# Optimization experiments

Measured on AMD Instinct MI355X. Metric: run time of the kernel, lower is better.

The kernel has to match this reference:

```python
import jax, jax.numpy as jnp
import numpy as np

NUM_PIXELS, B, C, H, A = 4096, 64, 512, 512, 256


def setup_inputs() -> dict:
    key = jax.random.key(0)
    ks = jax.random.split(key, 8)
    s = 0.02
    return {
        "keys": jax.random.normal(ks[0], (NUM_PIXELS, B, C), jnp.float32),
        "queries": jax.random.normal(ks[1], (1, B, H), jnp.float32),
        "Wa_w": jax.random.normal(ks[2], (A, C), jnp.float32) * s,
        "Wa_b": jax.random.normal(ks[3], (A,), jnp.float32) * s,
        "Ua_w": jax.random.normal(ks[4], (A, H), jnp.float32) * s,
        "Ua_b": jax.random.normal(ks[5], (A,), jnp.float32) * s,
        "va_w": jax.random.normal(ks[6], (1, A), jnp.float32) * s,
        "va_b": jax.random.normal(ks[7], (1,), jnp.float32) * s,
    }


def reference(keys, queries, Wa_w, Wa_b, Ua_w, Ua_b, va_w, va_b):
    # attn1: [P, B, A]; attn2: [1, B, A]
    attn1 = jnp.einsum("pbc,ac->pba", keys, Wa_w) + Wa_b
    attn2 = jnp.einsum("qbh,ah->qba", queries, Ua_w) + Ua_b
    # scores: [P, B] (va projects attn_size -> 1)
    scores = jnp.einsum("pba,a->pb", jnp.tanh(attn1 + attn2), va_w[0]) + va_b[0]
    weights = jax.nn.softmax(scores, axis=0)[..., None]  # [P, B, 1]
    context = jnp.sum(weights * keys, axis=0, keepdims=True)  # [1, B, C]
    return (context, weights)
```

## Files before the change

kernel.cpp:

```cpp
#include <hip/hip_runtime.h>
#include <cstdint>

#define CC 512
#define AA 256

typedef __bf16 bf16x8 __attribute__((ext_vector_type(8)));
typedef float f32x16 __attribute__((ext_vector_type(16)));

__device__ __forceinline__ unsigned short f2bf(float f) {
  union { float f; uint32_t u; } v; v.f = f;
  uint32_t r = (v.u + 0x7FFFu + ((v.u >> 16) & 1u)) >> 16;
  return (unsigned short)r;
}

__global__ void prep_kernel(const float* __restrict__ q,
                            const float* __restrict__ Wa_w,
                            const float* __restrict__ Wa_b,
                            const float* __restrict__ Ua_w,
                            const float* __restrict__ Ua_b,
                            unsigned short* __restrict__ wa_bf,
                            float* __restrict__ attn2,
                            float* __restrict__ out_ctx) {
  const int blk = blockIdx.x, t = threadIdx.x;
  if (blk < 64) {
    const int b = blk, a = t;
    float acc = Ua_b[a] + Wa_b[a];
    const float4* qr = (const float4*)(q + (size_t)b * CC);
    const float4* ur = (const float4*)(Ua_w + (size_t)a * CC);
#pragma unroll 4
    for (int i = 0; i < CC / 4; ++i) {
      float4 uu = ur[i]; float4 qq = qr[i];
      acc += uu.x * qq.x + uu.y * qq.y + uu.z * qq.z + uu.w * qq.w;
    }
    attn2[b * AA + a] = acc;
  } else if (blk < 128) {
    const int base = (blk - 64) * 2048 + t * 8;
#pragma unroll
    for (int i = 0; i < 8; ++i) wa_bf[base + i] = f2bf(Wa_w[base + i]);
  } else {
    const int base = (blk - 128) * 512 + t * 2;
    out_ctx[base] = 0.f; out_ctx[base + 1] = 0.f;
  }
}

__global__ __launch_bounds__(256, 2) void scores_kernel(
    const float* __restrict__ keys,
    const unsigned short* __restrict__ wa_bf,
    const float* __restrict__ attn2,
    const float* __restrict__ va_w,
    const float* __restrict__ va_b,
    float* __restrict__ scores) {
  __shared__ __align__(16) unsigned char smem[55296];
  unsigned short* As = (unsigned short*)smem;
  unsigned short* Bs = As + 128 * 72;

  const int t = threadIdx.x;
  const int w = t >> 6, lane = t & 63;
  const int m32 = lane & 31, kg = lane >> 5;
  const int R0w = (w & 1) * 64, C0w = (w >> 1) * 128;
  const long r0 = (long)blockIdx.x * 128;

  f32x16 acc[2][4];
#pragma unroll
  for (int i = 0; i < 2; ++i)
#pragma unroll
    for (int j = 0; j < 4; ++j)
#pragma unroll
      for (int e = 0; e < 16; ++e) acc[i][j][e] = 0.f;

  const int c4 = t & 15, rg = t >> 4;
  const int kq = t & 7, ng = t >> 3;

  for (int ko = 0; ko < 8; ++ko) {
    const int kb = ko * 64;
#pragma unroll
    for (int ps = 0; ps < 8; ++ps) {
      const int row = rg + ps * 16;
      float4 v = *(const float4*)(keys + (r0 + row) * CC + kb + c4 * 4);
      ushort4 h;
      h.x = f2bf(v.x); h.y = f2bf(v.y); h.z = f2bf(v.z); h.w = f2bf(v.w);
      *(ushort4*)(As + row * 72 + c4 * 4) = h;
    }
#pragma unroll
    for (int ps = 0; ps < 8; ++ps) {
      const int n = ng + ps * 32;
      int4 v = *(const int4*)(wa_bf + (size_t)n * CC + kb + kq * 8);
      *(int4*)(Bs + n * 72 + kq * 8) = v;
    }
    __syncthreads();
    for (int kk = 0; kk < 4; ++kk) {
      const int k0 = kk * 16 + kg * 8;
      bf16x8 a0 = *(const bf16x8*)(As + (R0w + m32) * 72 + k0);
      bf16x8 a1 = *(const bf16x8*)(As + (R0w + 32 + m32) * 72 + k0);
      bf16x8 b0 = *(const bf16x8*)(Bs + (C0w + m32) * 72 + k0);
      bf16x8 b1 = *(const bf16x8*)(Bs + (C0w + 32 + m32) * 72 + k0);
      bf16x8 b2 = *(const bf16x8*)(Bs + (C0w + 64 + m32) * 72 + k0);
      bf16x8 b3 = *(const bf16x8*)(Bs + (C0w + 96 + m32) * 72 + k0);
      acc[0][0] = __builtin_amdgcn_mfma_f32_32x32x16_bf16(a0, b0, acc[0][0], 0, 0, 0);
      acc[0][1] = __builtin_amdgcn_mfma_f32_32x32x16_bf16(a0, b1, acc[0][1], 0, 0, 0);
      acc[0][2] = __builtin_amdgcn_mfma_f32_32x32x16_bf16(a0, b2, acc[0][2], 0, 0, 0);
      acc[0][3] = __builtin_amdgcn_mfma_f32_32x32x16_bf16(a0, b3, acc[0][3], 0, 0, 0);
      acc[1][0] = __builtin_amdgcn_mfma_f32_32x32x16_bf16(a1, b0, acc[1][0], 0, 0, 0);
      acc[1][1] = __builtin_amdgcn_mfma_f32_32x32x16_bf16(a1, b1, acc[1][1], 0, 0, 0);
      acc[1][2] = __builtin_amdgcn_mfma_f32_32x32x16_bf16(a1, b2, acc[1][2], 0, 0, 0);
      acc[1][3] = __builtin_amdgcn_mfma_f32_32x32x16_bf16(a1, b3, acc[1][3], 0, 0, 0);
    }
    __syncthreads();
  }

  float* sc0 = (float*)smem;
  float* sc1 = sc0 + 128;

#pragma unroll
  for (int mt = 0; mt < 2; ++mt) {
    float ps[16];
#pragma unroll
    for (int r = 0; r < 16; ++r) ps[r] = 0.f;
    const int rowb = R0w + mt * 32 + 4 * kg;
#pragma unroll
    for (int nt = 0; nt < 4; ++nt) {
      const int col = C0w + nt * 32 + m32;
      const float vv = va_w[col];
#pragma unroll
      for (int r = 0; r < 16; ++r) {
        const int row = rowb + (r & 3) + 8 * (r >> 2);
        float x = acc[mt][nt][r] + attn2[(row & 63) * AA + col];
        float ax = fabsf(x);
        float e2 = __expf(-2.f * ax);
        float th = (1.f - e2) / (1.f + e2);
        ps[r] += copysignf(th, x) * vv;
      }
    }
#pragma unroll
    for (int off = 1; off <= 16; off <<= 1)
#pragma unroll
      for (int r = 0; r < 16; ++r) ps[r] += __shfl_xor(ps[r], off);
    if (m32 == 0) {
      float* dst = (w >> 1) ? sc1 : sc0;
#pragma unroll
      for (int r = 0; r < 16; ++r) dst[rowb + (r & 3) + 8 * (r >> 2)] = ps[r];
    }
  }
  __syncthreads();
  if (t < 128) scores[r0 + t] = sc0[t] + sc1[t] + va_b[0];
}

__global__ void softmax_kernel(const float* __restrict__ scores,
                               float* __restrict__ out) {
  const int b = blockIdx.x, t = threadIdx.x;
  const int w = t >> 6, lane = t & 63;
  __shared__ float red[4];
  float s[16];
  float m = -1e30f;
#pragma unroll
  for (int i = 0; i < 16; ++i) {
    s[i] = scores[(size_t)(t + 256 * i) * 64 + b];
    m = fmaxf(m, s[i]);
  }
#pragma unroll
  for (int off = 1; off <= 32; off <<= 1) m = fmaxf(m, __shfl_xor(m, off));
  if (lane == 0) red[w] = m;
  __syncthreads();
  m = fmaxf(fmaxf(red[0], red[1]), fmaxf(red[2], red[3]));
  float sum = 0.f;
#pragma unroll
  for (int i = 0; i < 16; ++i) { s[i] = __expf(s[i] - m); sum += s[i]; }
#pragma unroll
  for (int off = 1; off <= 32; off <<= 1) sum += __shfl_xor(sum, off);
  __syncthreads();
  if (lane == 0) red[w] = sum;
  __syncthreads();
  const float invZ = 1.f / (red[0] + red[1] + red[2] + red[3]);
  float* wout = out + 32768;
#pragma unroll
  for (int i = 0; i < 16; ++i)
    wout[(size_t)(t + 256 * i) * 64 + b] = s[i] * invZ;
}

__global__ __launch_bounds__(128) void context_kernel(
    const float* __restrict__ keys,
    const float* __restrict__ wts,
    float* __restrict__ out_ctx) {
  const int b = blockIdx.y, pc = blockIdx.x, t = threadIdx.x;
  const int p0 = pc * 128;
  __shared__ float wl[128];
  wl[t] = wts[(size_t)(p0 + t) * 64 + b];
  __syncthreads();
  float4 acc = {0.f, 0.f, 0.f, 0.f};
  const float4* kp = (const float4*)keys;
#pragma unroll 4
  for (int j = 0; j < 128; ++j) {
    float4 kv = kp[(size_t)((p0 + j) * 64 + b) * 128 + t];
    const float wj = wl[j];
    acc.x += wj * kv.x; acc.y += wj * kv.y;
    acc.z += wj * kv.z; acc.w += wj * kv.w;
  }
  float* dst = out_ctx + b * 512 + t * 4;
  atomicAdd(dst + 0, acc.x);
  atomicAdd(dst + 1, acc.y);
  atomicAdd(dst + 2, acc.z);
  atomicAdd(dst + 3, acc.w);
}

extern "C" void kernel_launch(void* const* d_in, const int* in_sizes, int n_in,
                              void* d_out, int out_size, void* d_ws, size_t ws_size,
                              hipStream_t stream) {
  (void)in_sizes; (void)n_in; (void)out_size; (void)ws_size;
  const float* keys = (const float*)d_in[0];
  const float* q    = (const float*)d_in[1];
  const float* Wa_w = (const float*)d_in[2];
  const float* Wa_b = (const float*)d_in[3];
  const float* Ua_w = (const float*)d_in[4];
  const float* Ua_b = (const float*)d_in[5];
  const float* va_w = (const float*)d_in[6];
  const float* va_b = (const float*)d_in[7];
  float* out = (float*)d_out;

  unsigned short* wa_bf = (unsigned short*)d_ws;
  float* attn2  = (float*)((char*)d_ws + 262144);
  float* scores = (float*)((char*)d_ws + 262144 + 65536);

  prep_kernel<<<192, 256, 0, stream>>>(q, Wa_w, Wa_b, Ua_w, Ua_b, wa_bf, attn2, out);
  scores_kernel<<<2048, 256, 0, stream>>>(keys, wa_bf, attn2, va_w, va_b, scores);
  softmax_kernel<<<64, 256, 0, stream>>>(scores, out);
  context_kernel<<<dim3(32, 64), 128, 0, stream>>>(keys, out + 32768, out);
}
```

Measured before the change: 849.8 us.

## Fuse scores, unnormalized softmax and context accumulation into one persistent pass

Merges the score GEMM, exponentiation and weighted context sum into a single kernel. Each of 256 blocks processes 8 row tiles and accumulates per-block context partials while the keys are still hot, replacing the separate max-softmax and second full read of keys. The max subtraction is dropped and exp(score) is used directly, which relies on scores staying small enough not to overflow. The trade-offs are a 64-float per-thread register accumulator, a 32 MB partial buffer that needs a reduce pass, and 512-thread blocks with only 256 blocks.

Result: slower. 960.6 us (+13.0%).

```diff
diff --git a/kernel.cpp b/kernel.cpp
--- a/kernel.cpp
+++ b/kernel.cpp
@@ -3,14 +3,15 @@
 
 #define CC 512
 #define AA 256
+#define NBLK 256
+#define TPB 8
 
 typedef __bf16 bf16x8 __attribute__((ext_vector_type(8)));
 typedef float f32x16 __attribute__((ext_vector_type(16)));
 
 __device__ __forceinline__ unsigned short f2bf(float f) {
   union { float f; uint32_t u; } v; v.f = f;
-  uint32_t r = (v.u + 0x7FFFu + ((v.u >> 16) & 1u)) >> 16;
-  return (unsigned short)r;
+  return (unsigned short)((v.u + 0x7FFFu + ((v.u >> 16) & 1u)) >> 16);
 }
 
 __global__ void prep_kernel(const float* __restrict__ q,
@@ -19,8 +20,7 @@
                             const float* __restrict__ Ua_w,
                             const float* __restrict__ Ua_b,
                             unsigned short* __restrict__ wa_bf,
-                            float* __restrict__ attn2,
-                            float* __restrict__ out_ctx) {
+                            float* __restrict__ attn2) {
   const int blk = blockIdx.x, t = threadIdx.x;
   if (blk < 64) {
     const int b = blk, a = t;
@@ -29,177 +29,192 @@
     const float4* ur = (const float4*)(Ua_w + (size_t)a * CC);
 #pragma unroll 4
     for (int i = 0; i < CC / 4; ++i) {
-      float4 uu = ur[i]; float4 qq = qr[i];
+      float4 uu = ur[i], qq = qr[i];
       acc += uu.x * qq.x + uu.y * qq.y + uu.z * qq.z + uu.w * qq.w;
     }
     attn2[b * AA + a] = acc;
-  } else if (blk < 128) {
+  } else {
     const int base = (blk - 64) * 2048 + t * 8;
 #pragma unroll
     for (int i = 0; i < 8; ++i) wa_bf[base + i] = f2bf(Wa_w[base + i]);
-  } else {
-    const int base = (blk - 128) * 512 + t * 2;
-    out_ctx[base] = 0.f; out_ctx[base + 1] = 0.f;
-  }
-}
-
-__global__ __launch_bounds__(256, 2) void scores_kernel(
+  }
+}
+
+__global__ __launch_bounds__(512, 2) void fused_kernel(
     const float* __restrict__ keys,
     const unsigned short* __restrict__ wa_bf,
     const float* __restrict__ attn2,
     const float* __restrict__ va_w,
     const float* __restrict__ va_b,
-    float* __restrict__ scores) {
-  __shared__ __align__(16) unsigned char smem[55296];
-  unsigned short* As = (unsigned short*)smem;
-  unsigned short* Bs = As + 128 * 72;
+    float* __restrict__ u_g,
+    float* __restrict__ cpart,
+    float* __restrict__ zpart) {
+  __shared__ __align__(16) unsigned short As[128 * 72];
+  __shared__ __align__(16) unsigned short Bs[256 * 72];
+  __shared__ float sc[4][128];
+  __shared__ __align__(16) float u_s[128];
+  __shared__ float zp_s[64];
 
   const int t = threadIdx.x;
-  const int w = t >> 6, lane = t & 63;
-  const int m32 = lane & 31, kg = lane >> 5;
-  const int R0w = (w & 1) * 64, C0w = (w >> 1) * 128;
-  const long r0 = (long)blockIdx.x * 128;
-
-  f32x16 acc[2][4];
-#pragma unroll
-  for (int i = 0; i < 2; ++i)
-#pragma unroll
-    for (int j = 0; j < 4; ++j)
-#pragma unroll
-      for (int e = 0; e < 16; ++e) acc[i][j][e] = 0.f;
+  const int w = t >> 6, lane = t & 63, m32 = lane & 31, kg = lane >> 5;
+  const int R0w = (w & 1) * 64, C0w = (w >> 1) * 64;
+
+  float Cown[64];
+#pragma unroll
+  for (int b = 0; b < 64; ++b) Cown[b] = 0.f;
+  if (t < 64) zp_s[t] = 0.f;
+  __syncthreads();
 
   const int c4 = t & 15, rg = t >> 4;
   const int kq = t & 7, ng = t >> 3;
 
-  for (int ko = 0; ko < 8; ++ko) {
-    const int kb = ko * 64;
-#pragma unroll
-    for (int ps = 0; ps < 8; ++ps) {
-      const int row = rg + ps * 16;
-      float4 v = *(const float4*)(keys + (r0 + row) * CC + kb + c4 * 4);
-      ushort4 h;
-      h.x = f2bf(v.x); h.y = f2bf(v.y); h.z = f2bf(v.z); h.w = f2bf(v.w);
-      *(ushort4*)(As + row * 72 + c4 * 4) = h;
-    }
-#pragma unroll
-    for (int ps = 0; ps < 8; ++ps) {
-      const int n = ng + ps * 32;
-      int4 v = *(const int4*)(wa_bf + (size_t)n * CC + kb + kq * 8);
-      *(int4*)(Bs + n * 72 + kq * 8) = v;
+  for (int tile = 0; tile < TPB; ++tile) {
+    const long r0 = ((long)blockIdx.x * TPB + tile) * 128;
+
+    f32x16 acc[2][2];
+#pragma unroll
+    for (int i = 0; i < 2; ++i)
+#pragma unroll
+      for (int j = 0; j < 2; ++j)
+#pragma unroll
+        for (int e = 0; e < 16; ++e) acc[i][j][e] = 0.f;
+
+    for (int ko = 0; ko < 8; ++ko) {
+      const int kb = ko * 64;
+#pragma unroll
+      for (int ps = 0; ps < 4; ++ps) {
+        const int row = rg + ps * 32;
+        float4 v = *(const float4*)(keys + (size_t)(r0 + row) * CC + kb + c4 * 4);
+        ushort4 h;
+        h.x = f2bf(v.x); h.y = f2bf(v.y); h.z = f2bf(v.z); h.w = f2bf(v.w);
+        *(ushort4*)(As + row * 72 + c4 * 4) = h;
+      }
+#pragma unroll
+      for (int ps = 0; ps < 4; ++ps) {
+        const int n = ng + ps * 64;
+        int4 v = *(const int4*)(wa_bf + (size_t)n * CC + kb + kq * 8);
+        *(int4*)(Bs + n * 72 + kq * 8) = v;
+      }
+      __syncthreads();
+#pragma unroll
+      for (int kk = 0; kk < 4; ++kk) {
+        const int k0 = kk * 16 + kg * 8;
+        bf16x8 a0 = *(const bf16x8*)(As + (R0w + m32) * 72 + k0);
+        bf16x8 a1 = *(const bf16x8*)(As + (R0w + 32 + m32) * 72 + k0);
+        bf16x8 b0 = *(const bf16x8*)(Bs + (C0w + m32) * 72 + k0);
+        bf16x8 b1 = *(const bf16x8*)(Bs + (C0w + 32 + m32) * 72 + k0);
+        acc[0][0] = __builtin_amdgcn_mfma_f32_32x32x16_bf16(a0, b0, acc[0][0], 0, 0, 0);
+        acc[0][1] = __builtin_amdgcn_mfma_f32_32x32x16_bf16(a0, b1, acc[0][1], 0, 0, 0);
+        acc[1][0] = __builtin_amdgcn_mfma_f32_32x32x16_bf16(a1, b0, acc[1][0], 0, 0, 0);
+        acc[1][1] = __builtin_amdgcn_mfma_f32_32x32x16_bf16(a1, b1, acc[1][1], 0, 0, 0);
+      }
+      __syncthreads();
+    }
+
+#pragma unroll
+    for (int mt = 0; mt < 2; ++mt) {
+      float ps_[16];
+#pragma unroll
+      for (int r = 0; r < 16; ++r) ps_[r] = 0.f;
+      const int rowb = R0w + mt * 32 + 4 * kg;
+#pragma unroll
+      for (int nt = 0; nt < 2; ++nt) {
+        const int col = C0w + nt * 32 + m32;
+        const float vv = va_w[col];
+#pragma unroll
+        for (int r = 0; r < 16; ++r) {
+          const int row = rowb + (r & 3) + 8 * (r >> 2);
+          float x = acc[mt][nt][r] + attn2[(row & 63) * AA + col];
+          float ax = fabsf(x);
+          float e2 = __expf(-2.f * ax);
+          float th = (1.f - e2) / (1.f + e2);
+          ps_[r] += copysignf(th, x) * vv;
+        }
+      }
+#pragma unroll
+      for (int off = 1; off <= 16; off <<= 1)
+#pragma unroll
+        for (int r = 0; r < 16; ++r) ps_[r] += __shfl_xor(ps_[r], off);
+      if (m32 == 0) {
+#pragma unroll
+        for (int r = 0; r < 16; ++r)
+          sc[w >> 1][rowb + (r & 3) + 8 * (r >> 2)] = ps_[r];
+      }
     }
     __syncthreads();
-    for (int kk = 0; kk < 4; ++kk) {
-      const int k0 = kk * 16 + kg * 8;
-      bf16x8 a0 = *(const bf16x8*)(As + (R0w + m32) * 72 + k0);
-      bf16x8 a1 = *(const bf16x8*)(As + (R0w + 32 + m32) * 72 + k0);
-      bf16x8 b0 = *(const bf16x8*)(Bs + (C0w + m32) * 72 + k0);
-      bf16x8 b1 = *(const bf16x8*)(Bs + (C0w + 32 + m32) * 72 + k0);
-      bf16x8 b2 = *(const bf16x8*)(Bs + (C0w + 64 + m32) * 72 + k0);
-      bf16x8 b3 = *(const bf16x8*)(Bs + (C0w + 96 + m32) * 72 + k0);
-      acc[0][0] = __builtin_amdgcn_mfma_f32_32x32x16_bf16(a0, b0, acc[0][0], 0, 0, 0);
-      acc[0][1] = __builtin_amdgcn_mfma_f32_32x32x16_bf16(a0, b1, acc[0][1], 0, 0, 0);
-      acc[0][2] = __builtin_amdgcn_mfma_f32_32x32x16_bf16(a0, b2, acc[0][2], 0, 0, 0);
-      acc[0][3] = __builtin_amdgcn_mfma_f32_32x32x16_bf16(a0, b3, acc[0][3], 0, 0, 0);
-      acc[1][0] = __builtin_amdgcn_mfma_f32_32x32x16_bf16(a1, b0, acc[1][0], 0, 0, 0);
-      acc[1][1] = __builtin_amdgcn_mfma_f32_32x32x16_bf16(a1, b1, acc[1][1], 0, 0, 0);
-      acc[1][2] = __builtin_amdgcn_mfma_f32_32x32x16_bf16(a1, b2, acc[1][2], 0, 0, 0);
-      acc[1][3] = __builtin_amdgcn_mfma_f32_32x32x16_bf16(a1, b3, acc[1][3], 0, 0, 0);
+    if (t < 64) {
+      float s0 = sc[0][t] + sc[1][t] + sc[2][t] + sc[3][t] + va_b[0];
+      float s1 = sc[0][t + 64] + sc[1][t + 64] + sc[2][t + 64] + sc[3][t + 64] + va_b[0];
+      float e0 = __expf(s0), e1 = __expf(s1);
+      u_s[t] = e0; u_s[t + 64] = e1;
+      u_g[r0 + t] = e0; u_g[r0 + 64 + t] = e1;
+      zp_s[t] += e0 + e1;
     }
     __syncthreads();
-  }
-
-  float* sc0 = (float*)smem;
-  float* sc1 = sc0 + 128;
-
-#pragma unroll
-  for (int mt = 0; mt < 2; ++mt) {
-    float ps[16];
-#pragma unroll
-    for (int r = 0; r < 16; ++r) ps[r] = 0.f;
-    const int rowb = R0w + mt * 32 + 4 * kg;
-#pragma unroll
-    for (int nt = 0; nt < 4; ++nt) {
-      const int col = C0w + nt * 32 + m32;
-      const float vv = va_w[col];
-#pragma unroll
-      for (int r = 0; r < 16; ++r) {
-        const int row = rowb + (r & 3) + 8 * (r >> 2);
-        float x = acc[mt][nt][r] + attn2[(row & 63) * AA + col];
-        float ax = fabsf(x);
-        float e2 = __expf(-2.f * ax);
-        float th = (1.f - e2) / (1.f + e2);
-        ps[r] += copysignf(th, x) * vv;
-      }
-    }
-#pragma unroll
-    for (int off = 1; off <= 16; off <<= 1)
-#pragma unroll
-      for (int r = 0; r < 16; ++r) ps[r] += __shfl_xor(ps[r], off);
-    if (m32 == 0) {
-      float* dst = (w >> 1) ? sc1 : sc0;
-#pragma unroll
-      for (int r = 0; r < 16; ++r) dst[rowb + (r & 3) + 8 * (r >> 2)] = ps[r];
-    }
-  }
-  __syncthreads();
-  if (t < 128) scores[r0 + t] = sc0[t] + sc1[t] + va_b[0];
-}
-
-__global__ void softmax_kernel(const float* __restrict__ scores,
-                               float* __restrict__ out) {
-  const int b = blockIdx.x, t = threadIdx.x;
-  const int w = t >> 6, lane = t & 63;
-  __shared__ float red[4];
-  float s[16];
-  float m = -1e30f;
-#pragma unroll
-  for (int i = 0; i < 16; ++i) {
-    s[i] = scores[(size_t)(t + 256 * i) * 64 + b];
-    m = fmaxf(m, s[i]);
-  }
-#pragma unroll
-  for (int off = 1; off <= 32; off <<= 1) m = fmaxf(m, __shfl_xor(m, off));
-  if (lane == 0) red[w] = m;
-  __syncthreads();
-  m = fmaxf(fmaxf(red[0], red[1]), fmaxf(red[2], red[3]));
-  float sum = 0.f;
-#pragma unroll
-  for (int i = 0; i < 16; ++i) { s[i] = __expf(s[i] - m); sum += s[i]; }
-#pragma unroll
-  for (int off = 1; off <= 32; off <<= 1) sum += __shfl_xor(sum, off);
-  __syncthreads();
-  if (lane == 0) red[w] = sum;
-  __syncthreads();
-  const float invZ = 1.f / (red[0] + red[1] + red[2] + red[3]);
-  float* wout = out + 32768;
-#pragma unroll
-  for (int i = 0; i < 16; ++i)
-    wout[(size_t)(t + 256 * i) * 64 + b] = s[i] * invZ;
-}
-
-__global__ __launch_bounds__(128) void context_kernel(
-    const float* __restrict__ keys,
-    const float* __restrict__ wts,
-    float* __restrict__ out_ctx) {
-  const int b = blockIdx.y, pc = blockIdx.x, t = threadIdx.x;
-  const int p0 = pc * 128;
-  __shared__ float wl[128];
-  wl[t] = wts[(size_t)(p0 + t) * 64 + b];
-  __syncthreads();
-  float4 acc = {0.f, 0.f, 0.f, 0.f};
-  const float4* kp = (const float4*)keys;
-#pragma unroll 4
-  for (int j = 0; j < 128; ++j) {
-    float4 kv = kp[(size_t)((p0 + j) * 64 + b) * 128 + t];
-    const float wj = wl[j];
-    acc.x += wj * kv.x; acc.y += wj * kv.y;
-    acc.z += wj * kv.z; acc.w += wj * kv.w;
-  }
-  float* dst = out_ctx + b * 512 + t * 4;
-  atomicAdd(dst + 0, acc.x);
-  atomicAdd(dst + 1, acc.y);
-  atomicAdd(dst + 2, acc.z);
-  atomicAdd(dst + 3, acc.w);
+
+    const float* krow = keys + (size_t)r0 * CC + t;
+#pragma unroll
+    for (int b4 = 0; b4 < 16; ++b4) {
+      float4 ua = *(const float4*)&u_s[b4 * 4];
+      float4 ub = *(const float4*)&u_s[b4 * 4 + 64];
+      const float* uap = (const float*)&ua;
+      const float* ubp = (const float*)&ub;
+#pragma unroll
+      for (int j = 0; j < 4; ++j) {
+        const int b = b4 * 4 + j;
+        float k0v = krow[(size_t)b * CC];
+        float k1v = krow[(size_t)(b + 64) * CC];
+        Cown[b] += uap[j] * k0v + ubp[j] * k1v;
+      }
+    }
+  }
+
+  const size_t base = (size_t)blockIdx.x * 32768;
+#pragma unroll
+  for (int b = 0; b < 64; ++b) cpart[base + b * 512 + t] = Cown[b];
+  if (t < 64) zpart[blockIdx.x * 64 + t] = zp_s[t];
+}
+
+__global__ void reduce_kernel(const float* __restrict__ cpart,
+                              const float* __restrict__ zpart,
+                              float* __restrict__ csum,
+                              float* __restrict__ zsum) {
+  const int t = threadIdx.x;
+  if (blockIdx.x < 128) {
+    const int j = blockIdx.x * 256 + t;
+    float s = 0.f;
+#pragma unroll 8
+    for (int k = 0; k < NBLK; ++k) s += cpart[(size_t)k * 32768 + j];
+    csum[j] = s;
+  } else if (t < 64) {
+    float s = 0.f;
+#pragma unroll 8
+    for (int k = 0; k < NBLK; ++k) s += zpart[k * 64 + t];
+    zsum[t] = s;
+  }
+}
+
+__global__ void finalize_kernel(const float* __restrict__ csum,
+                                const float* __restrict__ zsum,
+                                const float* __restrict__ u_g,
+                                float* __restrict__ out) {
+  const int gid = blockIdx.x * 256 + threadIdx.x;
+  const int j = gid * 4;
+  if (j < 32768) {
+    const int b = j >> 9;
+    const float invZ = 1.f / zsum[b];
+    float4 c = *(const float4*)(csum + j);
+    c.x *= invZ; c.y *= invZ; c.z *= invZ; c.w *= invZ;
+    *(float4*)(out + j) = c;
+  } else {
+    const int r = j - 32768;
+    float4 uu = *(const float4*)(u_g + r);
+    float4 zz = *(const float4*)(zsum + (r & 63));
+    float4 ww;
+    ww.x = uu.x / zz.x; ww.y = uu.y / zz.y;
+    ww.z = uu.z / zz.z; ww.w = uu.w / zz.w;
+    *(float4*)(out + 32768 + r) = ww;
+  }
 }
 
 extern "C" void kernel_launch(void* const* d_in, const int* in_sizes, int n_in,
@@ -217,11 +232,16 @@
   float* out = (float*)d_out;
 
   unsigned short* wa_bf = (unsigned short*)d_ws;
-  float* attn2  = (float*)((char*)d_ws + 262144);
-  float* scores = (float*)((char*)d_ws + 262144 + 65536);
-
-  prep_kernel<<<192, 256, 0, stream>>>(q, Wa_w, Wa_b, Ua_w, Ua_b, wa_bf, attn2, out);
-  scores_kernel<<<2048, 256, 0, stream>>>(keys, wa_bf, attn2, va_w, va_b, scores);
-  softmax_kernel<<<64, 256, 0, stream>>>(scores, out);
-  context_kernel<<<dim3(32, 64), 128, 0, stream>>>(keys, out + 32768, out);
-}
+  float* attn2 = (float*)((char*)d_ws + 262144);
+  float* u_g   = (float*)((char*)d_ws + 327680);
+  float* cpart = (float*)((char*)d_ws + 1376256);
+  float* zpart = (float*)((char*)d_ws + 34930688);
+  float* csum  = (float*)((char*)d_ws + 34996224);
+  float* zsum  = (float*)((char*)d_ws + 35127296);
+
+  prep_kernel<<<128, 256, 0, stream>>>(q, Wa_w, Wa_b, Ua_w, Ua_b, wa_bf, attn2);
+  fused_kernel<<<NBLK, 512, 0, stream>>>(keys, wa_bf, attn2, va_w, va_b,
+                                         u_g, cpart, zpart);
+  reduce_kernel<<<129, 256, 0, stream>>>(cpart, zpart, csum, zsum);
+  finalize_kernel<<<288, 256, 0, stream>>>(csum, zsum, u_g, out);
+}
```
